# Kernel optimization log

Hardware: AMD Instinct MI355X
Metric: run time of the kernel (lower is better)

Reference implementation:

```python
import jax, jax.numpy as jnp
import numpy as np

ROPE_BASE = 10000.0
NUM_HEADS = 16
NUM_KV_HEADS = 4


def _rms_norm(x, eps):
    # F.rms_norm with no weight: x / sqrt(mean(x^2) + eps)
    return x * jax.lax.rsqrt(jnp.mean(x * x, axis=-1, keepdims=True) + eps)


def _apply_rope(x, cos, sin):
    h = x.shape[-1] // 2
    x1, x2 = x[..., :h], x[..., h:]
    return jnp.concatenate([x1 * cos + x2 * sin, -x1 * sin + x2 * cos], axis=-1)


def setup_inputs() -> dict:
    key = jax.random.key(0)
    ks = jax.random.split(key, 5)
    B, T, D = 2, 2048, 1024
    H, Hkv = NUM_HEADS, NUM_KV_HEADS
    hd = D // H
    kv_dim = Hkv * hd
    s_in = 1.0 / np.sqrt(D)
    return {
        "x": jax.random.normal(ks[0], (B, T, D), dtype=jnp.float32),
        "Wq": jax.random.normal(ks[1], (D, D), dtype=jnp.float32) * s_in,
        "Wk": jax.random.normal(ks[2], (kv_dim, D), dtype=jnp.float32) * s_in,
        "Wv": jax.random.normal(ks[3], (kv_dim, D), dtype=jnp.float32) * s_in,
        "Wproj": jax.random.normal(ks[4], (D, D), dtype=jnp.float32) * s_in,
        "q_gain": jnp.full((H,), 1.0, dtype=jnp.float32),
    }


def reference(x, Wq, Wk, Wv, Wproj, q_gain):
    B, T, D = x.shape
    H, Hkv = NUM_HEADS, NUM_KV_HEADS
    hd = D // H
    rep = H // Hkv
    eps = jnp.finfo(x.dtype).eps

    # QKV projections (F.linear: x @ W.T)
    q = jnp.einsum('btd,od->bto', x, Wq).reshape(B, T, H, hd).transpose(0, 2, 1, 3)
    k = jnp.einsum('btd,od->bto', x, Wk).reshape(B, T, Hkv, hd).transpose(0, 2, 1, 3)
    v = jnp.einsum('btd,od->bto', x, Wv).reshape(B, T, Hkv, hd).transpose(0, 2, 1, 3)

    q = _rms_norm(q, eps)
    k = _rms_norm(k, eps)

    # RoPE tables: [1, 1, T, hd/2]
    inv_freq = 1.0 / (ROPE_BASE ** (jnp.arange(0, hd, 2, dtype=jnp.float32) / hd))
    f = jnp.arange(T, dtype=jnp.float32)[:, None] * inv_freq[None, :]
    cos = jnp.cos(f)[None, None].astype(q.dtype)
    sin = jnp.sin(f)[None, None].astype(q.dtype)
    q = _apply_rope(q, cos, sin)
    k = _apply_rope(k, cos, sin)

    q = q * q_gain.astype(q.dtype)[None, :, None, None]

    # GQA without materializing repeated K/V: group q heads [Hkv, rep]
    qg = q.reshape(B, Hkv, rep, T, hd)
    scale = hd ** -0.5
    scores = jnp.einsum('bgrqd,bgkd->bgrqk', qg, k) * scale
    causal = jnp.tril(jnp.ones((T, T), dtype=bool))
    scores = jnp.where(causal, scores, -jnp.inf)
    att = jax.nn.softmax(scores.astype(jnp.float32), axis=-1).astype(q.dtype)
    y = jnp.einsum('bgrqk,bgkd->bgrqd', att, v)  # [B,Hkv,rep,T,hd]
    y = y.reshape(B, H, T, hd).transpose(0, 2, 1, 3).reshape(B, T, D)
    return jnp.einsum('btd,od->bto', y, Wproj)
```

## Files before the change

### kernel.cpp

```cpp
#include <hip/hip_runtime.h>
#include <cstdint>
#include <cstddef>

typedef __attribute__((ext_vector_type(8))) short short8;
typedef __attribute__((ext_vector_type(4))) float floatx4;
typedef __attribute__((ext_vector_type(4))) short short4v;
typedef unsigned short u16;
typedef unsigned int u32;

#define B_   2
#define T_   2048
#define D_   1024
#define H_   16
#define HKV_ 4
#define HD_  64
#define KV_  256
#define M_   4096
#define QS_  1536

#define NX   4194304
#define NWQ  1048576
#define NWK  262144
#define NWV  262144
#define NWP  1048576
#define NCAST (NX + NWQ + NWK + NWV + NWP)
#define CAST_BLOCKS (NCAST / 1024)
#define TAB_BLOCKS  256

__device__ __forceinline__ float b2f(u16 u) {
    union { u32 i; float f; } v; v.i = ((u32)u) << 16; return v.f;
}
__device__ __forceinline__ u16 f2b(float f) {
    union { float f; u32 i; } v; v.f = f;
    u32 r = v.i + 0x7FFF + ((v.i >> 16) & 1);
    return (u16)(r >> 16);
}
__device__ __forceinline__ u32 pack_hi(float a, float b) {
    union { float f; u32 u; } ua, ub; ua.f = a; ub.f = b;
    return (ua.u >> 16) | (ub.u & 0xFFFF0000u);
}

__device__ __forceinline__ void async16(const u16* g, u16* l) {
    __builtin_amdgcn_global_load_lds(
        (const __attribute__((address_space(1))) u32*)g,
        (__attribute__((address_space(3))) u32*)l, 16, 0, 0);
}

__global__ __launch_bounds__(256) void prep(const float* __restrict__ x,
                                            const float* __restrict__ wq,
                                            const float* __restrict__ wk,
                                            const float* __restrict__ wv,
                                            const float* __restrict__ wp,
                                            u16* __restrict__ dst,
                                            float2* __restrict__ tab) {
    int blk = blockIdx.x;
    if (blk < CAST_BLOCKS) {
        int i = blk * 1024 + threadIdx.x * 4;
        const float* src; int off;
        if      (i < NX)                  { src = x;  off = i; }
        else if (i < NX+NWQ)              { src = wq; off = i - NX; }
        else if (i < NX+NWQ+NWK)          { src = wk; off = i - (NX+NWQ); }
        else if (i < NX+NWQ+NWK+NWV)      { src = wv; off = i - (NX+NWQ+NWK); }
        else                              { src = wp; off = i - (NX+NWQ+NWK+NWV); }
        float4 v = *(const float4*)(src + off);
        short4v o;
        o.x = (short)f2b(v.x); o.y = (short)f2b(v.y);
        o.z = (short)f2b(v.z); o.w = (short)f2b(v.w);
        *(short4v*)(dst + i) = o;
    } else {
        int idx = (blk - CAST_BLOCKS) * 256 + threadIdx.x;
        int t = idx >> 5, i = idx & 31;
        float freq = exp2f(-(float)i * (13.287712379549449f / 32.0f));
        float ang = (float)t * freq;
        tab[idx] = make_float2(cosf(ang), sinf(ang));
    }
}

__global__ __launch_bounds__(256) void gemm_qkv(const u16* __restrict__ A,
                                                const u16* __restrict__ W,
                                                u16* __restrict__ C,
                                                u16* __restrict__ Vt,
                                                const float* __restrict__ gain,
                                                const float2* __restrict__ tab) {
    const int K = D_;
    __shared__ u16 As[2][128 * 32];
    __shared__ u16 Bs[2][128 * 32];
    const int t = threadIdx.x;
    const int wave = t >> 6, lane = t & 63;
    const int quad = lane >> 4, l16 = lane & 15;
    const int wm = (wave >> 1) * 64, wn = (wave & 1) * 64;
    const int m0 = blockIdx.y * 128, n0 = blockIdx.x * 128;

    floatx4 acc[4][4];
#pragma unroll
    for (int i = 0; i < 4; i++)
#pragma unroll
        for (int j = 0; j < 4; j++) acc[i][j] = (floatx4){0.f, 0.f, 0.f, 0.f};

    const int sr = t >> 2, sc = (t & 3) * 8;
    const u16* ga = A + (size_t)(m0 + sr) * K + sc;
    const u16* gb = W + (size_t)(n0 + sr) * K + sc;

    async16(ga, As[0] + t * 8);
    async16(ga + (size_t)64 * K, As[0] + t * 8 + 64 * 32);
    async16(gb, Bs[0] + t * 8);
    async16(gb + (size_t)64 * K, Bs[0] + t * 8 + 64 * 32);

    int cur = 0;
    for (int kt = 0; kt < K; kt += 32) {
        __syncthreads();
        if (kt + 32 < K) {
            const u16* ga2 = ga + kt + 32;
            const u16* gb2 = gb + kt + 32;
            u16* lA = As[cur ^ 1] + t * 8;
            u16* lB = Bs[cur ^ 1] + t * 8;
            async16(ga2, lA);
            async16(ga2 + (size_t)64 * K, lA + 64 * 32);
            async16(gb2, lB);
            async16(gb2 + (size_t)64 * K, lB + 64 * 32);
        }
        short8 af[4], bf[4];
#pragma unroll
        for (int mt = 0; mt < 4; mt++)
            af[mt] = *(const short8*)(As[cur] + (wm + mt * 16 + l16) * 32 + quad * 8);
#pragma unroll
        for (int nt = 0; nt < 4; nt++)
            bf[nt] = *(const short8*)(Bs[cur] + (wn + nt * 16 + l16) * 32 + quad * 8);
#pragma unroll
        for (int mt = 0; mt < 4; mt++)
#pragma unroll
            for (int nt = 0; nt < 4; nt++)
                acc[mt][nt] = __builtin_amdgcn_mfma_f32_16x16x32_bf16(
                    af[mt], bf[nt], acc[mt][nt], 0, 0, 0);
        cur ^= 1;
    }

    const int col0 = n0 + wn;
    if (col0 < 1280) {
        float gs = (col0 < 1024)
                 ? gain[col0 >> 6] * (0.125f * 1.4426950408889634f)
                 : 1.0f;
#pragma unroll
        for (int mt = 0; mt < 4; mt++)
#pragma unroll
            for (int r = 0; r < 4; r++) {
                int row = m0 + wm + mt * 16 + quad * 4 + r;
                int tt = row & (T_ - 1);
                float v0 = acc[mt][0][r], v1 = acc[mt][1][r];
                float v2 = acc[mt][2][r], v3 = acc[mt][3][r];
                float ss = v0 * v0 + v1 * v1 + v2 * v2 + v3 * v3;
                ss += __shfl_xor(ss, 1); ss += __shfl_xor(ss, 2);
                ss += __shfl_xor(ss, 4); ss += __shfl_xor(ss, 8);
                float inv = rsqrtf(ss * (1.0f / 64.0f) + 1.1920929e-7f);
                v0 *= inv; v1 *= inv; v2 *= inv; v3 *= inv;
                float2 cs0 = tab[tt * 32 + l16];
                float2 cs1 = tab[tt * 32 + 16 + l16];
                float o0 = (v0 * cs0.x + v2 * cs0.y) * gs;
                float o1 = (v1 * cs1.x + v3 * cs1.y) * gs;
                float o2 = (v2 * cs0.x - v0 * cs0.y) * gs;
                float o3 = (v3 * cs1.x - v1 * cs1.y) * gs;
                u16* cp = C + (size_t)row * QS_ + col0 + l16;
                cp[0]  = f2b(o0);
                cp[16] = f2b(o1);
                cp[32] = f2b(o2);
                cp[48] = f2b(o3);
            }
    } else {
        const int g = (col0 - 1280) >> 6;
#pragma unroll
        for (int mt = 0; mt < 4; mt++)
#pragma unroll
            for (int r = 0; r < 4; r++) {
                int row = m0 + wm + mt * 16 + quad * 4 + r;
                int tt = row & (T_ - 1);
                int bb = row >> 11;
#pragma unroll
                for (int nt = 0; nt < 4; nt++)
                    Vt[(size_t)((bb * 4 + g) * 64 + nt * 16 + l16) * T_ + tt] =
                        f2b(acc[mt][nt][r]);
            }
    }
}

template <typename OutT>
__global__ __launch_bounds__(256) void gemm128(const u16* __restrict__ A,
                                               const u16* __restrict__ W,
                                               OutT* __restrict__ C,
                                               int M, int N, int K, int ldc) {
    __shared__ u16 As[2][128 * 32];
    __shared__ u16 Bs[2][128 * 32];
    const int t = threadIdx.x;
    const int wave = t >> 6, lane = t & 63;
    const int quad = lane >> 4, l16 = lane & 15;
    const int wm = (wave >> 1) * 64, wn = (wave & 1) * 64;
    const int m0 = blockIdx.y * 128, n0 = blockIdx.x * 128;

    floatx4 acc[4][4];
#pragma unroll
    for (int i = 0; i < 4; i++)
#pragma unroll
        for (int j = 0; j < 4; j++) acc[i][j] = (floatx4){0.f, 0.f, 0.f, 0.f};

    const int sr = t >> 2, sc = (t & 3) * 8;
    const u16* ga = A + (size_t)(m0 + sr) * K + sc;
    const u16* gb = W + (size_t)(n0 + sr) * K + sc;

    async16(ga, As[0] + t * 8);
    async16(ga + (size_t)64 * K, As[0] + t * 8 + 64 * 32);
    async16(gb, Bs[0] + t * 8);
    async16(gb + (size_t)64 * K, Bs[0] + t * 8 + 64 * 32);

    int cur = 0;
    for (int kt = 0; kt < K; kt += 32) {
        __syncthreads();
        if (kt + 32 < K) {
            const u16* ga2 = ga + kt + 32;
            const u16* gb2 = gb + kt + 32;
            u16* lA = As[cur ^ 1] + t * 8;
            u16* lB = Bs[cur ^ 1] + t * 8;
            async16(ga2, lA);
            async16(ga2 + (size_t)64 * K, lA + 64 * 32);
            async16(gb2, lB);
            async16(gb2 + (size_t)64 * K, lB + 64 * 32);
        }
        short8 af[4], bf[4];
#pragma unroll
        for (int mt = 0; mt < 4; mt++)
            af[mt] = *(const short8*)(As[cur] + (wm + mt * 16 + l16) * 32 + quad * 8);
#pragma unroll
        for (int nt = 0; nt < 4; nt++)
            bf[nt] = *(const short8*)(Bs[cur] + (wn + nt * 16 + l16) * 32 + quad * 8);
#pragma unroll
        for (int mt = 0; mt < 4; mt++)
#pragma unroll
            for (int nt = 0; nt < 4; nt++)
                acc[mt][nt] = __builtin_amdgcn_mfma_f32_16x16x32_bf16(
                    af[mt], bf[nt], acc[mt][nt], 0, 0, 0);
        cur ^= 1;
    }

#pragma unroll
    for (int mt = 0; mt < 4; mt++)
#pragma unroll
        for (int nt = 0; nt < 4; nt++)
#pragma unroll
            for (int r = 0; r < 4; r++) {
                int row = m0 + wm + mt * 16 + quad * 4 + r;
                int col = n0 + wn + nt * 16 + l16;
                float val = acc[mt][nt][r];
                if constexpr (sizeof(OutT) == 4) C[(size_t)row * ldc + col] = val;
                else                             C[(size_t)row * ldc + col] = (OutT)f2b(val);
            }
}

__global__ __launch_bounds__(256) void flash(const u16* __restrict__ QKV,
                                             const u16* __restrict__ Vtr,
                                             u16* __restrict__ Y) {
    const int xp = blockIdx.x;
    const int h  = blockIdx.y;
    const int b  = blockIdx.z;
    const int g  = h >> 2;
    const int w    = threadIdx.x >> 6;
    const int lane = threadIdx.x & 63;
    const int quad = lane >> 4, l16 = lane & 15;

    __shared__ u16 Kt[2][64 * 64];
    __shared__ u16 Vs[2][64 * 64];
    __shared__ __align__(16) u16 P[4][2][16][72];

    const int mA = xp * 64 + w * 16;
    const int mB = (31 - xp) * 64 + w * 16;
    const int nA = xp + 1;
    const int nB = 32 - xp;

    const u16* qpA = QKV + (size_t)(b * T_ + mA + l16) * QS_ + h * HD_ + quad * 8;
    const u16* qpB = QKV + (size_t)(b * T_ + mB + l16) * QS_ + h * HD_ + quad * 8;
    short8 aqA0 = *(const short8*)(qpA);
    short8 aqA1 = *(const short8*)(qpA + 32);
    short8 aqB0 = *(const short8*)(qpB);
    short8 aqB1 = *(const short8*)(qpB + 32);

    short8 ones;
#pragma unroll
    for (int i = 0; i < 8; i++) ones[i] = (short)0x3F80;

    floatx4 accA[4], accB[4];
#pragma unroll
    for (int i = 0; i < 4; i++) {
        accA[i] = (floatx4){0.f, 0.f, 0.f, 0.f};
        accB[i] = (floatx4){0.f, 0.f, 0.f, 0.f};
    }
    floatx4 lAcc = (floatx4){0.f, 0.f, 0.f, 0.f};
    floatx4 lBcc = (floatx4){0.f, 0.f, 0.f, 0.f};

    const int srow = w * 16 + (lane >> 3);
    const int sseg = (lane & 7) ^ ((lane >> 3) & 7);
    const u16* kg = QKV + (size_t)(b * T_ + srow) * QS_ + D_ + g * 64 + sseg * 8;
    const u16* vg = Vtr + (size_t)((b * 4 + g) * 64 + srow) * T_ + sseg * 8;

    const int sw0 = (quad ^ (l16 & 7)) * 8;
    const int sw1 = ((4 + quad) ^ (l16 & 7)) * 8;

    async16(kg, Kt[0] + w * 1024 + lane * 8);
    async16(kg + (size_t)8 * QS_, Kt[0] + w * 1024 + lane * 8 + 512);
    async16(vg, Vs[0] + w * 1024 + lane * 8);
    async16(vg + (size_t)8 * T_, Vs[0] + w * 1024 + lane * 8 + 512);

    int cur = 0;
    for (int tk = 0; tk < nB; tk++) {
        const bool dual = (tk < nA);
        __syncthreads();
        if (tk + 1 < nB) {
            kg += (size_t)64 * QS_;
            vg += 64;
            u16* klds = Kt[cur ^ 1] + w * 1024 + lane * 8;
            u16* vlds = Vs[cur ^ 1] + w * 1024 + lane * 8;
            async16(kg, klds);
            async16(kg + (size_t)8 * QS_, klds + 512);
            async16(vg, vlds);
            async16(vg + (size_t)8 * T_, vlds + 512);
        }

        floatx4 SB[4], SA[4];
#pragma unroll
        for (int nt = 0; nt < 4; nt++) {
            const u16* kr = Kt[cur] + (nt * 16 + l16) * 64;
            short8 kf0 = *(const short8*)(kr + sw0);
            short8 kf1 = *(const short8*)(kr + sw1);
            SB[nt] = (floatx4){0.f, 0.f, 0.f, 0.f};
            SB[nt] = __builtin_amdgcn_mfma_f32_16x16x32_bf16(kf0, aqB0, SB[nt], 0, 0, 0);
            SB[nt] = __builtin_amdgcn_mfma_f32_16x16x32_bf16(kf1, aqB1, SB[nt], 0, 0, 0);
            if (dual) {
                SA[nt] = (floatx4){0.f, 0.f, 0.f, 0.f};
                SA[nt] = __builtin_amdgcn_mfma_f32_16x16x32_bf16(kf0, aqA0, SA[nt], 0, 0, 0);
                SA[nt] = __builtin_amdgcn_mfma_f32_16x16x32_bf16(kf1, aqA1, SA[nt], 0, 0, 0);
            }
        }
        short8 vf[4][2];
#pragma unroll
        for (int dd = 0; dd < 4; dd++) {
            const u16* vr = Vs[cur] + (dd * 16 + l16) * 64;
            vf[dd][0] = *(const short8*)(vr + sw0);
            vf[dd][1] = *(const short8*)(vr + sw1);
        }

        const bool maskB = (tk == nB - 1);
        const int qB = mB + l16;
#pragma unroll
        for (int nt = 0; nt < 4; nt++) {
            float p[4];
#pragma unroll
            for (int r = 0; r < 4; r++) {
                float e = __builtin_amdgcn_exp2f(SB[nt][r]);
                if (maskB) {
                    int key = tk * 64 + nt * 16 + quad * 4 + r;
                    e = (key <= qB) ? e : 0.f;
                }
                p[r] = e;
            }
            uint2 pw; pw.x = pack_hi(p[0], p[1]); pw.y = pack_hi(p[2], p[3]);
            *(uint2*)&P[w][1][l16][nt * 16 + quad * 4] = pw;
        }
        short8 pfB0 = *(const short8*)&P[w][1][l16][quad * 8];
        short8 pfB1 = *(const short8*)&P[w][1][l16][quad * 8 + 32];
#pragma unroll
        for (int dd = 0; dd < 4; dd++) {
            accB[dd] = __builtin_amdgcn_mfma_f32_16x16x32_bf16(pfB0, vf[dd][0], accB[dd], 0, 0, 0);
            accB[dd] = __builtin_amdgcn_mfma_f32_16x16x32_bf16(pfB1, vf[dd][1], accB[dd], 0, 0, 0);
        }
        lBcc = __builtin_amdgcn_mfma_f32_16x16x32_bf16(pfB0, ones, lBcc, 0, 0, 0);
        lBcc = __builtin_amdgcn_mfma_f32_16x16x32_bf16(pfB1, ones, lBcc, 0, 0, 0);

        if (dual) {
            const bool maskA = (tk == nA - 1);
            const int qA = mA + l16;
#pragma unroll
            for (int nt = 0; nt < 4; nt++) {
                float p[4];
#pragma unroll
                for (int r = 0; r < 4; r++) {
                    float e = __builtin_amdgcn_exp2f(SA[nt][r]);
                    if (maskA) {
                        int key = tk * 64 + nt * 16 + quad * 4 + r;
                        e = (key <= qA) ? e : 0.f;
                    }
                    p[r] = e;
                }
                uint2 pw; pw.x = pack_hi(p[0], p[1]); pw.y = pack_hi(p[2], p[3]);
                *(uint2*)&P[w][0][l16][nt * 16 + quad * 4] = pw;
            }
            short8 pfA0 = *(const short8*)&P[w][0][l16][quad * 8];
            short8 pfA1 = *(const short8*)&P[w][0][l16][quad * 8 + 32];
#pragma unroll
            for (int dd = 0; dd < 4; dd++) {
                accA[dd] = __builtin_amdgcn_mfma_f32_16x16x32_bf16(pfA0, vf[dd][0], accA[dd], 0, 0, 0);
                accA[dd] = __builtin_amdgcn_mfma_f32_16x16x32_bf16(pfA1, vf[dd][1], accA[dd], 0, 0, 0);
            }
            lAcc = __builtin_amdgcn_mfma_f32_16x16x32_bf16(pfA0, ones, lAcc, 0, 0, 0);
            lAcc = __builtin_amdgcn_mfma_f32_16x16x32_bf16(pfA1, ones, lAcc, 0, 0, 0);
        }
        cur ^= 1;
    }

#pragma unroll
    for (int r = 0; r < 4; r++) {
        float invA = 1.0f / lAcc[r];
        float invB = 1.0f / lBcc[r];
        int rowA = mA + quad * 4 + r;
        int rowB = mB + quad * 4 + r;
        u16* ypA = Y + (size_t)(b * T_ + rowA) * D_ + h * HD_ + l16;
        u16* ypB = Y + (size_t)(b * T_ + rowB) * D_ + h * HD_ + l16;
#pragma unroll
        for (int dd = 0; dd < 4; dd++) {
            ypA[dd * 16] = f2b(accA[dd][r] * invA);
            ypB[dd * 16] = f2b(accB[dd][r] * invB);
        }
    }
}

extern "C" void kernel_launch(void* const* d_in, const int* in_sizes, int n_in,
                              void* d_out, int out_size, void* d_ws, size_t ws_size,
                              hipStream_t stream) {
    const float* x    = (const float*)d_in[0];
    const float* Wq   = (const float*)d_in[1];
    const float* Wk   = (const float*)d_in[2];
    const float* Wv   = (const float*)d_in[3];
    const float* Wp   = (const float*)d_in[4];
    const float* gain = (const float*)d_in[5];
    float* out = (float*)d_out;

    u16* xb   = (u16*)d_ws;
    u16* Wcat = xb + (size_t)NX;
    u16* Wpb  = Wcat + (size_t)(NWQ + NWK + NWV);
    u16* QKV  = Wpb + (size_t)NWP;
    u16* Vt   = QKV + (size_t)M_ * QS_;
    u16* Y    = Vt + (size_t)M_ * KV_;
    float2* tab = (float2*)(Y + (size_t)M_ * D_);

    prep<<<CAST_BLOCKS + TAB_BLOCKS, 256, 0, stream>>>(x, Wq, Wk, Wv, Wp, xb, tab);

    gemm_qkv<<<dim3(QS_ / 128, M_ / 128), 256, 0, stream>>>(xb, Wcat, QKV, Vt,
                                                            gain, tab);

    flash<<<dim3(16, H_, B_), 256, 0, stream>>>(QKV, Vt, Y);

    gemm128<float><<<dim3(D_ / 128, M_ / 128), 256, 0, stream>>>(Y, Wpb, out,
                                                                 M_, D_, D_, D_);
}
```

Before: 182.1 us.

## Shrink GEMM tiles to 128x64 and single-buffer flash K/V tiles

Both projection GEMMs move from 128x128 to 128x64 output tiles, with each wave owning a 32x64 strip, and add a launch-bounds occupancy hint of 3 blocks. This doubles the block count so more of the GPU is filled, at the cost of reloading A tiles more often. The flash kernel drops the double-buffered K/V LDS and instead issues the next tile load after fragments are read, with an extra barrier. That cuts LDS use to raise occupancy, but it exposes load latency that the double buffer used to hide.

```diff
diff --git a/kernel.cpp b/kernel.cpp
--- a/kernel.cpp
+++ b/kernel.cpp
@@ -76,24 +76,24 @@
     }
 }
 
-__global__ __launch_bounds__(256) void gemm_qkv(const u16* __restrict__ A,
-                                                const u16* __restrict__ W,
-                                                u16* __restrict__ C,
-                                                u16* __restrict__ Vt,
-                                                const float* __restrict__ gain,
-                                                const float2* __restrict__ tab) {
+__global__ __launch_bounds__(256, 3) void gemm_qkv(const u16* __restrict__ A,
+                                                   const u16* __restrict__ W,
+                                                   u16* __restrict__ C,
+                                                   u16* __restrict__ Vt,
+                                                   const float* __restrict__ gain,
+                                                   const float2* __restrict__ tab) {
     const int K = D_;
     __shared__ u16 As[2][128 * 32];
-    __shared__ u16 Bs[2][128 * 32];
+    __shared__ u16 Bs[2][64 * 32];
     const int t = threadIdx.x;
     const int wave = t >> 6, lane = t & 63;
     const int quad = lane >> 4, l16 = lane & 15;
-    const int wm = (wave >> 1) * 64, wn = (wave & 1) * 64;
-    const int m0 = blockIdx.y * 128, n0 = blockIdx.x * 128;
-
-    floatx4 acc[4][4];
-#pragma unroll
-    for (int i = 0; i < 4; i++)
+    const int wm = wave * 32;
+    const int m0 = blockIdx.y * 128, n0 = blockIdx.x * 64;
+
+    floatx4 acc[2][4];
+#pragma unroll
+    for (int i = 0; i < 2; i++)
 #pragma unroll
         for (int j = 0; j < 4; j++) acc[i][j] = (floatx4){0.f, 0.f, 0.f, 0.f};
 
@@ -104,7 +104,6 @@
     async16(ga, As[0] + t * 8);
     async16(ga + (size_t)64 * K, As[0] + t * 8 + 64 * 32);
     async16(gb, Bs[0] + t * 8);
-    async16(gb + (size_t)64 * K, Bs[0] + t * 8 + 64 * 32);
 
     int cur = 0;
     for (int kt = 0; kt < K; kt += 32) {
@@ -112,22 +111,19 @@
         if (kt + 32 < K) {
             const u16* ga2 = ga + kt + 32;
             const u16* gb2 = gb + kt + 32;
-            u16* lA = As[cur ^ 1] + t * 8;
-            u16* lB = Bs[cur ^ 1] + t * 8;
-            async16(ga2, lA);
-            async16(ga2 + (size_t)64 * K, lA + 64 * 32);
-            async16(gb2, lB);
-            async16(gb2 + (size_t)64 * K, lB + 64 * 32);
-        }
-        short8 af[4], bf[4];
-#pragma unroll
-        for (int mt = 0; mt < 4; mt++)
+            async16(ga2, As[cur ^ 1] + t * 8);
+            async16(ga2 + (size_t)64 * K, As[cur ^ 1] + t * 8 + 64 * 32);
+            async16(gb2, Bs[cur ^ 1] + t * 8);
+        }
+        short8 af[2], bf[4];
+#pragma unroll
+        for (int mt = 0; mt < 2; mt++)
             af[mt] = *(const short8*)(As[cur] + (wm + mt * 16 + l16) * 32 + quad * 8);
 #pragma unroll
         for (int nt = 0; nt < 4; nt++)
-            bf[nt] = *(const short8*)(Bs[cur] + (wn + nt * 16 + l16) * 32 + quad * 8);
-#pragma unroll
-        for (int mt = 0; mt < 4; mt++)
+            bf[nt] = *(const short8*)(Bs[cur] + (nt * 16 + l16) * 32 + quad * 8);
+#pragma unroll
+        for (int mt = 0; mt < 2; mt++)
 #pragma unroll
             for (int nt = 0; nt < 4; nt++)
                 acc[mt][nt] = __builtin_amdgcn_mfma_f32_16x16x32_bf16(
@@ -135,13 +131,13 @@
         cur ^= 1;
     }
 
-    const int col0 = n0 + wn;
+    const int col0 = n0;
     if (col0 < 1280) {
         float gs = (col0 < 1024)
                  ? gain[col0 >> 6] * (0.125f * 1.4426950408889634f)
                  : 1.0f;
 #pragma unroll
-        for (int mt = 0; mt < 4; mt++)
+        for (int mt = 0; mt < 2; mt++)
 #pragma unroll
             for (int r = 0; r < 4; r++) {
                 int row = m0 + wm + mt * 16 + quad * 4 + r;
@@ -168,7 +164,7 @@
     } else {
         const int g = (col0 - 1280) >> 6;
 #pragma unroll
-        for (int mt = 0; mt < 4; mt++)
+        for (int mt = 0; mt < 2; mt++)
 #pragma unroll
             for (int r = 0; r < 4; r++) {
                 int row = m0 + wm + mt * 16 + quad * 4 + r;
@@ -182,22 +178,21 @@
     }
 }
 
-template <typename OutT>
-__global__ __launch_bounds__(256) void gemm128(const u16* __restrict__ A,
-                                               const u16* __restrict__ W,
-                                               OutT* __restrict__ C,
-                                               int M, int N, int K, int ldc) {
+__global__ __launch_bounds__(256, 3) void gemm_proj(const u16* __restrict__ A,
+                                                    const u16* __restrict__ W,
+                                                    float* __restrict__ C) {
+    const int K = D_;
     __shared__ u16 As[2][128 * 32];
-    __shared__ u16 Bs[2][128 * 32];
+    __shared__ u16 Bs[2][64 * 32];
     const int t = threadIdx.x;
     const int wave = t >> 6, lane = t & 63;
     const int quad = lane >> 4, l16 = lane & 15;
-    const int wm = (wave >> 1) * 64, wn = (wave & 1) * 64;
-    const int m0 = blockIdx.y * 128, n0 = blockIdx.x * 128;
-
-    floatx4 acc[4][4];
-#pragma unroll
-    for (int i = 0; i < 4; i++)
+    const int wm = wave * 32;
+    const int m0 = blockIdx.y * 128, n0 = blockIdx.x * 64;
+
+    floatx4 acc[2][4];
+#pragma unroll
+    for (int i = 0; i < 2; i++)
 #pragma unroll
         for (int j = 0; j < 4; j++) acc[i][j] = (floatx4){0.f, 0.f, 0.f, 0.f};
 
@@ -208,7 +203,6 @@
     async16(ga, As[0] + t * 8);
     async16(ga + (size_t)64 * K, As[0] + t * 8 + 64 * 32);
     async16(gb, Bs[0] + t * 8);
-    async16(gb + (size_t)64 * K, Bs[0] + t * 8 + 64 * 32);
 
     int cur = 0;
     for (int kt = 0; kt < K; kt += 32) {
@@ -216,22 +210,19 @@
         if (kt + 32 < K) {
             const u16* ga2 = ga + kt + 32;
             const u16* gb2 = gb + kt + 32;
-            u16* lA = As[cur ^ 1] + t * 8;
-            u16* lB = Bs[cur ^ 1] + t * 8;
-            async16(ga2, lA);
-            async16(ga2 + (size_t)64 * K, lA + 64 * 32);
-            async16(gb2, lB);
-            async16(gb2 + (size_t)64 * K, lB + 64 * 32);
-        }
-        short8 af[4], bf[4];
-#pragma unroll
-        for (int mt = 0; mt < 4; mt++)
+            async16(ga2, As[cur ^ 1] + t * 8);
+            async16(ga2 + (size_t)64 * K, As[cur ^ 1] + t * 8 + 64 * 32);
+            async16(gb2, Bs[cur ^ 1] + t * 8);
+        }
+        short8 af[2], bf[4];
+#pragma unroll
+        for (int mt = 0; mt < 2; mt++)
             af[mt] = *(const short8*)(As[cur] + (wm + mt * 16 + l16) * 32 + quad * 8);
 #pragma unroll
         for (int nt = 0; nt < 4; nt++)
-            bf[nt] = *(const short8*)(Bs[cur] + (wn + nt * 16 + l16) * 32 + quad * 8);
-#pragma unroll
-        for (int mt = 0; mt < 4; mt++)
+            bf[nt] = *(const short8*)(Bs[cur] + (nt * 16 + l16) * 32 + quad * 8);
+#pragma unroll
+        for (int mt = 0; mt < 2; mt++)
 #pragma unroll
             for (int nt = 0; nt < 4; nt++)
                 acc[mt][nt] = __builtin_amdgcn_mfma_f32_16x16x32_bf16(
@@ -240,16 +231,14 @@
     }
 
 #pragma unroll
-    for (int mt = 0; mt < 4; mt++)
+    for (int mt = 0; mt < 2; mt++)
 #pragma unroll
         for (int nt = 0; nt < 4; nt++)
 #pragma unroll
             for (int r = 0; r < 4; r++) {
                 int row = m0 + wm + mt * 16 + quad * 4 + r;
-                int col = n0 + wn + nt * 16 + l16;
-                float val = acc[mt][nt][r];
-                if constexpr (sizeof(OutT) == 4) C[(size_t)row * ldc + col] = val;
-                else                             C[(size_t)row * ldc + col] = (OutT)f2b(val);
+                int col = n0 + nt * 16 + l16;
+                C[(size_t)row * D_ + col] = acc[mt][nt][r];
             }
 }
 
@@ -264,8 +253,8 @@
     const int lane = threadIdx.x & 63;
     const int quad = lane >> 4, l16 = lane & 15;
 
-    __shared__ u16 Kt[2][64 * 64];
-    __shared__ u16 Vs[2][64 * 64];
+    __shared__ u16 Kt[64 * 64];
+    __shared__ u16 Vs[64 * 64];
     __shared__ __align__(16) u16 P[4][2][16][72];
 
     const int mA = xp * 64 + w * 16;
@@ -297,34 +286,25 @@
     const int sseg = (lane & 7) ^ ((lane >> 3) & 7);
     const u16* kg = QKV + (size_t)(b * T_ + srow) * QS_ + D_ + g * 64 + sseg * 8;
     const u16* vg = Vtr + (size_t)((b * 4 + g) * 64 + srow) * T_ + sseg * 8;
+    u16* klds = Kt + w * 1024 + lane * 8;
+    u16* vlds = Vs + w * 1024 + lane * 8;
 
     const int sw0 = (quad ^ (l16 & 7)) * 8;
     const int sw1 = ((4 + quad) ^ (l16 & 7)) * 8;
 
-    async16(kg, Kt[0] + w * 1024 + lane * 8);
-    async16(kg + (size_t)8 * QS_, Kt[0] + w * 1024 + lane * 8 + 512);
-    async16(vg, Vs[0] + w * 1024 + lane * 8);
-    async16(vg + (size_t)8 * T_, Vs[0] + w * 1024 + lane * 8 + 512);
-
-    int cur = 0;
+    async16(kg, klds);
+    async16(kg + (size_t)8 * QS_, klds + 512);
+    async16(vg, vlds);
+    async16(vg + (size_t)8 * T_, vlds + 512);
+
     for (int tk = 0; tk < nB; tk++) {
         const bool dual = (tk < nA);
         __syncthreads();
-        if (tk + 1 < nB) {
-            kg += (size_t)64 * QS_;
-            vg += 64;
-            u16* klds = Kt[cur ^ 1] + w * 1024 + lane * 8;
-            u16* vlds = Vs[cur ^ 1] + w * 1024 + lane * 8;
-            async16(kg, klds);
-            async16(kg + (size_t)8 * QS_, klds + 512);
-            async16(vg, vlds);
-            async16(vg + (size_t)8 * T_, vlds + 512);
-        }
 
         floatx4 SB[4], SA[4];
 #pragma unroll
         for (int nt = 0; nt < 4; nt++) {
-            const u16* kr = Kt[cur] + (nt * 16 + l16) * 64;
+            const u16* kr = Kt + (nt * 16 + l16) * 64;
             short8 kf0 = *(const short8*)(kr + sw0);
             short8 kf1 = *(const short8*)(kr + sw1);
             SB[nt] = (floatx4){0.f, 0.f, 0.f, 0.f};
@@ -339,9 +319,18 @@
         short8 vf[4][2];
 #pragma unroll
         for (int dd = 0; dd < 4; dd++) {
-            const u16* vr = Vs[cur] + (dd * 16 + l16) * 64;
+            const u16* vr = Vs + (dd * 16 + l16) * 64;
             vf[dd][0] = *(const short8*)(vr + sw0);
             vf[dd][1] = *(const short8*)(vr + sw1);
+        }
+        __syncthreads();
+        if (tk + 1 < nB) {
+            kg += (size_t)64 * QS_;
+            vg += 64;
+            async16(kg, klds);
+            async16(kg + (size_t)8 * QS_, klds + 512);
+            async16(vg, vlds);
+            async16(vg + (size_t)8 * T_, vlds + 512);
         }
 
         const bool maskB = (tk == nB - 1);
@@ -399,7 +388,6 @@
             lAcc = __builtin_amdgcn_mfma_f32_16x16x32_bf16(pfA0, ones, lAcc, 0, 0, 0);
             lAcc = __builtin_amdgcn_mfma_f32_16x16x32_bf16(pfA1, ones, lAcc, 0, 0, 0);
         }
-        cur ^= 1;
     }
 
 #pragma unroll
@@ -439,11 +427,10 @@
 
     prep<<<CAST_BLOCKS + TAB_BLOCKS, 256, 0, stream>>>(x, Wq, Wk, Wv, Wp, xb, tab);
 
-    gemm_qkv<<<dim3(QS_ / 128, M_ / 128), 256, 0, stream>>>(xb, Wcat, QKV, Vt,
-                                                            gain, tab);
+    gemm_qkv<<<dim3(QS_ / 64, M_ / 128), 256, 0, stream>>>(xb, Wcat, QKV, Vt,
+                                                           gain, tab);
 
     flash<<<dim3(16, H_, B_), 256, 0, stream>>>(QKV, Vt, Y);
 
-    gemm128<float><<<dim3(D_ / 128, M_ / 128), 256, 0, stream>>>(Y, Wpb, out,
-                                                                 M_, D_, D_, D_);
-}
+    gemm_proj<<<dim3(D_ / 64, M_ / 128), 256, 0, stream>>>(Y, Wpb, out);
+}
```

New measurement: 174.1 us. 1.05x faster.
